# Kernel optimization log

Hardware: AMD Instinct MI355X
Metric: run time of the kernel (lower is better)

## Reference

```python
import jax, jax.numpy as jnp
import numpy as np

ALPHA = 0.0005
TAU = 0.2


def setup_inputs() -> dict:
    key = jax.random.key(0)
    k1, k2, k3 = jax.random.split(key, 3)
    output = jax.random.normal(k1, (8192, 1000), dtype=jnp.float32)
    target = jax.random.normal(k2, (8192, 1000), dtype=jnp.float32)
    conv_w = jax.random.normal(k3, (256, 256, 128, 3), dtype=jnp.float32)
    return {"output": output, "target": target, "conv_w": conv_w}


def reference(output, target, conv_w):
    # base loss (nn.MSELoss with default 'mean' reduction)
    loss = jnp.mean((output - target) ** 2)

    # Diversity regularizer: pairwise cosine similarity between slices
    # conv_w[:, :, i, :] along dim 2 ('filters' = size(2) in the original).
    F = conv_w.shape[2]
    # V: [F, D] with D = out_ch * in_ch * kw
    V = jnp.transpose(conv_w, (2, 0, 1, 3)).reshape(F, -1)
    norms = jnp.linalg.norm(V, axis=1)                      # [F]
    G = (V @ V.T) / (norms[:, None] * norms[None, :])       # [F, F] cosine Gram

    # keep entries with tau < sim <= 1 and i != j
    offdiag = ~jnp.eye(F, dtype=bool)
    mask = (G > TAU) & (G <= 1.0) & offdiag
    reg = jnp.sum(jnp.where(mask, G, jnp.zeros((), dtype=G.dtype)))

    return loss + ALPHA * reg
```

## Files before the change

kernel.cpp:

```cpp
#include <hip/hip_runtime.h>
#include <hip/hip_bf16.h>


typedef __attribute__((ext_vector_type(8))) short bf16x8;
typedef __attribute__((ext_vector_type(4))) float f32x4;

#define ALPHA 0.0005f
#define TAU 0.2f

#define FDIM 128
#define NGRAM 1024
#define NMSE 2048
#define NPAIRQ 8192
#define GRAM_ELEMS 16384
#define MSE_N4 2048000

__device__ __forceinline__ unsigned int pack_bf2(float lo, float hi) {
    union { float f; unsigned int u; } a, b;
    a.f = lo; b.f = hi;
    unsigned int al = (a.u + 0x7fffu + ((a.u >> 16) & 1u)) >> 16;
    unsigned int bh = (b.u + 0x7fffu + ((b.u >> 16) & 1u)) & 0xffff0000u;
    return (al & 0xffffu) | bh;
}

__device__ __forceinline__ bf16x8 make_frag(const float3& a, const float3& b) {
    union { bf16x8 v; unsigned int u[4]; } r;
    r.u[0] = pack_bf2(a.x, a.y);
    r.u[1] = pack_bf2(a.z, b.x);
    r.u[2] = pack_bf2(b.y, b.z);
    r.u[3] = 0;
    return r.v;
}

struct OctB { float3 B[8][2]; float3 A[2][2]; };

__device__ __forceinline__ void load_oct(const float* __restrict__ lp,
                                         const float* __restrict__ lpA,
                                         OctB& o) {
#pragma unroll
    for (int tt = 0; tt < 8; ++tt) {
        o.B[tt][0] = *reinterpret_cast<const float3*>(lp + tt * 48);
        o.B[tt][1] = *reinterpret_cast<const float3*>(lp + tt * 48 + 384);
    }
#pragma unroll
    for (int a = 0; a < 2; ++a) {
        o.A[a][0] = *reinterpret_cast<const float3*>(lpA + a * 48);
        o.A[a][1] = *reinterpret_cast<const float3*>(lpA + a * 48 + 384);
    }
    __builtin_amdgcn_sched_barrier(0);
}

__device__ __forceinline__ void consume_oct(const OctB& o,
                                            f32x4 (&acc0)[8], f32x4 (&acc1)[8]) {
    const bf16x8 fA0 = make_frag(o.A[0][0], o.A[0][1]);
    const bf16x8 fA1 = make_frag(o.A[1][0], o.A[1][1]);
#pragma unroll
    for (int cc = 0; cc < 8; ++cc) {
        const bf16x8 fb = make_frag(o.B[cc][0], o.B[cc][1]);
        acc0[cc] = __builtin_amdgcn_mfma_f32_16x16x32_bf16(fA0, fb, acc0[cc], 0, 0, 0);
        acc1[cc] = __builtin_amdgcn_mfma_f32_16x16x32_bf16(fA1, fb, acc1[cc], 0, 0, 0);
    }
}

__global__ void __launch_bounds__(256, 2) fused_kernel(
        const float* __restrict__ o, const float* __restrict__ t,
        const float* __restrict__ conv,
        float* __restrict__ mse_part, unsigned int* __restrict__ pp) {
    __shared__ float red[4];
    const int tid = threadIdx.x;
    const int lane = tid & 63;
    const int wave = tid >> 6;

    if (blockIdx.x >= NGRAM) {
        const int mb = blockIdx.x - NGRAM;
        const int gid = mb * 256 + tid;
        const f32x4* o4 = reinterpret_cast<const f32x4*>(o);
        const f32x4* t4 = reinterpret_cast<const f32x4*>(t);
        float s = 0.f;
#pragma unroll 4
        for (int i = gid; i < MSE_N4; i += NMSE * 256) {
            f32x4 a = o4[i], b = t4[i];
            f32x4 d = a - b;
            s += d[0]*d[0] + d[1]*d[1] + d[2]*d[2] + d[3]*d[3];
        }
        for (int off = 32; off; off >>= 1) s += __shfl_down(s, off);
        if (lane == 0) red[wave] = s;
        __syncthreads();
        if (tid == 0) mse_part[mb] = red[0] + red[1] + red[2] + red[3];
        return;
    }

    const int g = lane >> 4;
    const int fl = lane & 15;
    const float* lp  = conv + (size_t)blockIdx.x * 24576 + (2 * g) * 384 + fl * 3;
    const float* lpA = lp + wave * 96;

    f32x4 acc0[8], acc1[8];
#pragma unroll
    for (int cc = 0; cc < 8; ++cc) { acc0[cc] = (f32x4)0.f; acc1[cc] = (f32x4)0.f; }

    OctB O0, O1;
    load_oct(lp,        lpA,        O0);
    load_oct(lp + 3072, lpA + 3072, O1);

#pragma unroll
    for (int oo = 0; oo < 8; oo += 2) {
        consume_oct(O0, acc0, acc1);
        if (oo + 2 < 8) load_oct(lp + (oo + 2) * 3072, lpA + (oo + 2) * 3072, O0);
        consume_oct(O1, acc0, acc1);
        if (oo + 3 < 8) load_oct(lp + (oo + 3) * 3072, lpA + (oo + 3) * 3072, O1);
    }

    unsigned int* myp = pp + (size_t)blockIdx.x * NPAIRQ;
    const int rsub = (lane >> 4) << 2;
#pragma unroll
    for (int cc = 0; cc < 8; ++cc) {
        const int col = cc * 16 + fl;
#pragma unroll
        for (int j = 0; j < 4; ++j) {
            const int pr = wave * 16 + rsub + j;
            myp[pr * FDIM + col] = pack_bf2(acc0[cc][j], acc1[cc][j]);
        }
    }
}

__global__ void __launch_bounds__(256) reduce_kernel(
        const unsigned int* __restrict__ pp, float* __restrict__ gram) {
    __shared__ float red[16][16][2];
    const int tid = threadIdx.x;
    const int u = tid & 15;
    const int s = tid >> 4;
    const int qq = blockIdx.x * 16 + u;
    float lo = 0.f, hi = 0.f;
#pragma unroll 8
    for (int b = s * 64; b < s * 64 + 64; ++b) {
        const unsigned int v = pp[(size_t)b * NPAIRQ + qq];
        lo += __uint_as_float(v << 16);
        hi += __uint_as_float(v & 0xffff0000u);
    }
    red[s][u][0] = lo; red[s][u][1] = hi;
    __syncthreads();
    if (tid < 32) {
        const int u2 = tid >> 1, h = tid & 1;
        float x = 0.f;
#pragma unroll
        for (int s2 = 0; s2 < 16; ++s2) x += red[s2][u2][h];
        gram[(blockIdx.x * 16 + u2) * 2 + h] = x;
    }
}

__global__ void __launch_bounds__(256) finalize_kernel(
        const float* __restrict__ gram, const float* __restrict__ mse_part,
        float* __restrict__ out) {
    __shared__ float rn[FDIM];
    __shared__ float redS[4], redM[4];
    const int tid = threadIdx.x;
    if (tid < FDIM) {
        const int row = tid;
        const int pr = (row >> 5) * 16 + (row & 15);
        const int h = (row >> 4) & 1;
        rn[row] = rsqrtf(gram[(pr * FDIM + row) * 2 + h]);
    }
    __syncthreads();
    float s = 0.f;
    for (int i = tid; i < GRAM_ELEMS; i += 256) {
        const int h = i & 1;
        const int qq = i >> 1;
        const int col = qq & 127;
        const int pr = qq >> 7;
        const int row = (pr >> 4) * 32 + (pr & 15) + (h << 4);
        const float gv = gram[i] * rn[row] * rn[col];
        if (row != col && gv > TAU && gv <= 1.0f) s += gv;
    }
    float m = 0.f;
#pragma unroll 8
    for (int j = 0; j < 8; ++j) m += mse_part[tid * 8 + j];
    for (int off = 32; off; off >>= 1) {
        s += __shfl_down(s, off);
        m += __shfl_down(m, off);
    }
    if ((tid & 63) == 0) { redS[tid >> 6] = s; redM[tid >> 6] = m; }
    __syncthreads();
    if (tid == 0)
        out[0] = (redM[0] + redM[1] + redM[2] + redM[3]) * (1.0f / 8192000.0f) +
                 ALPHA * (redS[0] + redS[1] + redS[2] + redS[3]);
}

extern "C" void kernel_launch(void* const* d_in, const int* in_sizes, int n_in,
                              void* d_out, int out_size, void* d_ws, size_t ws_size,
                              hipStream_t stream) {
    const float* output = (const float*)d_in[0];
    const float* target = (const float*)d_in[1];
    const float* conv   = (const float*)d_in[2];
    float* out = (float*)d_out;

    float* wsf       = (float*)d_ws;
    float* mse_part  = wsf;
    float* gram      = wsf + NMSE;
    unsigned int* pp = (unsigned int*)(wsf + NMSE + GRAM_ELEMS);
    (void)ws_size;

    fused_kernel<<<NGRAM + NMSE, 256, 0, stream>>>(output, target, conv,
                                                   mse_part, pp);
    reduce_kernel<<<NPAIRQ / 16, 256, 0, stream>>>(pp, gram);
    finalize_kernel<<<1, 256, 0, stream>>>(gram, mse_part, out);
}
```

Baseline: 71.96 us.

## Stage conv slices through LDS as bf16 tile for full-K MFMA fragments

The Gram computation now loads conv weights with coalesced float4 reads, converts pairs to bf16 and transposes them into a padded shared-memory tile. MFMA fragments are then read from LDS with all 8 K-lanes filled, instead of building fragments from float3 register loads that left a quarter of each fragment zero. Gram blocks drop from 1024 to 512, each doing twice the work, and MSE blocks drop to 1536, with the reduce and finalize loop bounds changed to match. The cost is added LDS traffic and barriers per chunk, and fewer partial Gram buffers to sum.

```diff
diff --git a/kernel.cpp b/kernel.cpp
--- a/kernel.cpp
+++ b/kernel.cpp
@@ -9,10 +9,12 @@
 #define TAU 0.2f
 
 #define FDIM 128
-#define NGRAM 1024
-#define NMSE 2048
+#define TSTRIDE 52
+#define GRAM_NBLK 512
+#define NMSE 1536
+#define CHUNK_F4 3072
+#define GRAM_ELEMS 16384
 #define NPAIRQ 8192
-#define GRAM_ELEMS 16384
 #define MSE_N4 2048000
 
 __device__ __forceinline__ unsigned int pack_bf2(float lo, float hi) {
@@ -23,61 +25,42 @@
     return (al & 0xffffu) | bh;
 }
 
-__device__ __forceinline__ bf16x8 make_frag(const float3& a, const float3& b) {
-    union { bf16x8 v; unsigned int u[4]; } r;
-    r.u[0] = pack_bf2(a.x, a.y);
-    r.u[1] = pack_bf2(a.z, b.x);
-    r.u[2] = pack_bf2(b.y, b.z);
-    r.u[3] = 0;
-    return r.v;
-}
-
-struct OctB { float3 B[8][2]; float3 A[2][2]; };
-
-__device__ __forceinline__ void load_oct(const float* __restrict__ lp,
-                                         const float* __restrict__ lpA,
-                                         OctB& o) {
-#pragma unroll
-    for (int tt = 0; tt < 8; ++tt) {
-        o.B[tt][0] = *reinterpret_cast<const float3*>(lp + tt * 48);
-        o.B[tt][1] = *reinterpret_cast<const float3*>(lp + tt * 48 + 384);
-    }
-#pragma unroll
-    for (int a = 0; a < 2; ++a) {
-        o.A[a][0] = *reinterpret_cast<const float3*>(lpA + a * 48);
-        o.A[a][1] = *reinterpret_cast<const float3*>(lpA + a * 48 + 384);
-    }
-    __builtin_amdgcn_sched_barrier(0);
-}
-
-__device__ __forceinline__ void consume_oct(const OctB& o,
-                                            f32x4 (&acc0)[8], f32x4 (&acc1)[8]) {
-    const bf16x8 fA0 = make_frag(o.A[0][0], o.A[0][1]);
-    const bf16x8 fA1 = make_frag(o.A[1][0], o.A[1][1]);
-#pragma unroll
-    for (int cc = 0; cc < 8; ++cc) {
-        const bf16x8 fb = make_frag(o.B[cc][0], o.B[cc][1]);
-        acc0[cc] = __builtin_amdgcn_mfma_f32_16x16x32_bf16(fA0, fb, acc0[cc], 0, 0, 0);
-        acc1[cc] = __builtin_amdgcn_mfma_f32_16x16x32_bf16(fA1, fb, acc1[cc], 0, 0, 0);
-    }
-}
-
-__global__ void __launch_bounds__(256, 2) fused_kernel(
+__device__ __forceinline__ void mfmaph(const unsigned short* __restrict__ tu,
+                                       int wave, int colr, int hi8,
+                                       f32x4 (&acc0)[8], f32x4 (&acc1)[8]) {
+#pragma unroll
+    for (int ks = 0; ks < 3; ++ks) {
+        const int koff = ks * 32 + hi8;
+        bf16x8 a0 = *reinterpret_cast<const bf16x8*>(
+            &tu[(wave * 32 + colr) * (TSTRIDE * 2) + koff]);
+        bf16x8 a1 = *reinterpret_cast<const bf16x8*>(
+            &tu[(wave * 32 + 16 + colr) * (TSTRIDE * 2) + koff]);
+#pragma unroll
+        for (int cc = 0; cc < 8; ++cc) {
+            bf16x8 b = *reinterpret_cast<const bf16x8*>(
+                &tu[(cc * 16 + colr) * (TSTRIDE * 2) + koff]);
+            acc0[cc] = __builtin_amdgcn_mfma_f32_16x16x32_bf16(a0, b, acc0[cc], 0, 0, 0);
+            acc1[cc] = __builtin_amdgcn_mfma_f32_16x16x32_bf16(a1, b, acc1[cc], 0, 0, 0);
+        }
+    }
+}
+
+__global__ void __launch_bounds__(256, 4) fused_kernel(
         const float* __restrict__ o, const float* __restrict__ t,
         const float* __restrict__ conv,
         float* __restrict__ mse_part, unsigned int* __restrict__ pp) {
+    __shared__ unsigned int tile[FDIM * TSTRIDE];
     __shared__ float red[4];
     const int tid = threadIdx.x;
     const int lane = tid & 63;
     const int wave = tid >> 6;
 
-    if (blockIdx.x >= NGRAM) {
-        const int mb = blockIdx.x - NGRAM;
+    if (blockIdx.x >= GRAM_NBLK) {
+        const int mb = blockIdx.x - GRAM_NBLK;
         const int gid = mb * 256 + tid;
         const f32x4* o4 = reinterpret_cast<const f32x4*>(o);
         const f32x4* t4 = reinterpret_cast<const f32x4*>(t);
         float s = 0.f;
-#pragma unroll 4
         for (int i = gid; i < MSE_N4; i += NMSE * 256) {
             f32x4 a = o4[i], b = t4[i];
             f32x4 d = a - b;
@@ -90,32 +73,43 @@
         return;
     }
 
-    const int g = lane >> 4;
-    const int fl = lane & 15;
-    const float* lp  = conv + (size_t)blockIdx.x * 24576 + (2 * g) * 384 + fl * 3;
-    const float* lpA = lp + wave * 96;
+    const int p = tid >> 4;
+    const int q = tid & 15;
+    const int colr = lane & 15;
+    const int hi8 = (lane >> 4) * 8;
+    const unsigned short* tileu = reinterpret_cast<const unsigned short*>(tile);
 
     f32x4 acc0[8], acc1[8];
 #pragma unroll
     for (int cc = 0; cc < 8; ++cc) { acc0[cc] = (f32x4)0.f; acc1[cc] = (f32x4)0.f; }
 
-    OctB O0, O1;
-    load_oct(lp,        lpA,        O0);
-    load_oct(lp + 3072, lpA + 3072, O1);
-
-#pragma unroll
-    for (int oo = 0; oo < 8; oo += 2) {
-        consume_oct(O0, acc0, acc1);
-        if (oo + 2 < 8) load_oct(lp + (oo + 2) * 3072, lpA + (oo + 2) * 3072, O0);
-        consume_oct(O1, acc0, acc1);
-        if (oo + 3 < 8) load_oct(lp + (oo + 3) * 3072, lpA + (oo + 3) * 3072, O1);
+    const f32x4* src4 = reinterpret_cast<const f32x4*>(conv);
+    const size_t cb = (size_t)blockIdx.x * (4 * CHUNK_F4) + (2 * p) * 96 + q;
+
+    for (int c = 0; c < 4; ++c) {
+        __syncthreads();
+#pragma unroll
+        for (int it = 0; it < 6; ++it) {
+            const f32x4 v0 = src4[cb + c * CHUNK_F4 + 16 * it];
+            const f32x4 v1 = src4[cb + c * CHUNK_F4 + 96 + 16 * it];
+            const int off4 = q + 16 * it;
+#pragma unroll
+            for (int u = 0; u < 4; ++u) {
+                const int idx = off4 * 4 + u;
+                const int f = idx / 3;
+                const int k = idx - 3 * f;
+                tile[f * TSTRIDE + k * 16 + p] = pack_bf2(v0[u], v1[u]);
+            }
+        }
+        __syncthreads();
+        mfmaph(tileu, wave, colr, hi8, acc0, acc1);
     }
 
     unsigned int* myp = pp + (size_t)blockIdx.x * NPAIRQ;
     const int rsub = (lane >> 4) << 2;
 #pragma unroll
     for (int cc = 0; cc < 8; ++cc) {
-        const int col = cc * 16 + fl;
+        const int col = cc * 16 + colr;
 #pragma unroll
         for (int j = 0; j < 4; ++j) {
             const int pr = wave * 16 + rsub + j;
@@ -133,7 +127,7 @@
     const int qq = blockIdx.x * 16 + u;
     float lo = 0.f, hi = 0.f;
 #pragma unroll 8
-    for (int b = s * 64; b < s * 64 + 64; ++b) {
+    for (int b = s * 32; b < s * 32 + 32; ++b) {
         const unsigned int v = pp[(size_t)b * NPAIRQ + qq];
         lo += __uint_as_float(v << 16);
         hi += __uint_as_float(v & 0xffff0000u);
@@ -173,8 +167,8 @@
         if (row != col && gv > TAU && gv <= 1.0f) s += gv;
     }
     float m = 0.f;
-#pragma unroll 8
-    for (int j = 0; j < 8; ++j) m += mse_part[tid * 8 + j];
+#pragma unroll 6
+    for (int j = 0; j < 6; ++j) m += mse_part[tid * 6 + j];
     for (int off = 32; off; off >>= 1) {
         s += __shfl_down(s, off);
         m += __shfl_down(m, off);
@@ -200,8 +194,8 @@
     unsigned int* pp = (unsigned int*)(wsf + NMSE + GRAM_ELEMS);
     (void)ws_size;
 
-    fused_kernel<<<NGRAM + NMSE, 256, 0, stream>>>(output, target, conv,
-                                                   mse_part, pp);
+    fused_kernel<<<GRAM_NBLK + NMSE, 256, 0, stream>>>(output, target, conv,
+                                                       mse_part, pp);
     reduce_kernel<<<NPAIRQ / 16, 256, 0, stream>>>(pp, gram);
     finalize_kernel<<<1, 256, 0, stream>>>(gram, mse_part, out);
 }
```

Result: faster. 57.77 us (-19.7%).
